# Kernel optimization log

Measured on AMD Instinct MI355X. Metric: run time of the kernel, lower is better.

## Reference

```python
import jax, jax.numpy as jnp
import numpy as np

N = 32768
WORD_DIM, TAG_DIM, REL_DIM, MEM_DIM, AT_HID = 300, 20, 20, 150, 20
IN_LEAF = WORD_DIM + TAG_DIM                      # 320, input to leaf SimpleGRU
IN_NODE = WORD_DIM + MEM_DIM + REL_DIM + TAG_DIM  # 490, input to GRU_AT


def _build_tree(seed=0):
    rng = np.random.default_rng(seed)
    parent = np.zeros(N, np.int64)
    for i in range(1, N):
        parent[i] = rng.integers(max(0, i - 64), i)
    children = [[] for _ in range(N)]
    for i in range(1, N):
        children[parent[i]].append(i)
    # Edge schedule: parents in DECREASING index order, children ascending.
    # Since child index > parent index, all edges below a node fire before
    # the node itself is consumed as a child => same order as the Python
    # post-order recursion in the torch code.
    edges = []
    for p in range(N - 1, -1, -1):
        for c in children[p]:
            edges.append((p, c))
    edges = np.asarray(edges, np.int32)            # (N-1, 2)
    leaf_ids = np.asarray([i for i in range(N) if not children[i]], np.int32)
    return edges, leaf_ids


def setup_inputs() -> dict:
    key = jax.random.key(0)
    ks = jax.random.split(key, 16)
    s = 0.05
    edges, leaf_ids = _build_tree()
    return {
        "w_emb":  jax.random.normal(ks[0], (N, WORD_DIM), jnp.float32),
        "tag_emb": jax.random.normal(ks[1], (N, TAG_DIM), jnp.float32),
        "rel_emb": jax.random.normal(ks[2], (N, REL_DIM), jnp.float32),
        "leaf_h": jax.random.uniform(ks[3], (MEM_DIM,), jnp.float32),
        # leaf SimpleGRU: stacked [Wz,Wr,Wh], [Uz,Ur,Uh], combined bias bW+bU
        "leaf_W": jax.random.normal(ks[4], (3, MEM_DIM, IN_LEAF), jnp.float32) * s,
        "leaf_U": jax.random.normal(ks[5], (3, MEM_DIM, MEM_DIM), jnp.float32) * s,
        "leaf_b": jax.random.normal(ks[6], (3, MEM_DIM), jnp.float32) * s,
        # GRU_AT inner SimpleGRU
        "node_W": jax.random.normal(ks[7], (3, MEM_DIM, IN_NODE), jnp.float32) * s,
        "node_U": jax.random.normal(ks[8], (3, MEM_DIM, MEM_DIM), jnp.float32) * s,
        "node_b": jax.random.normal(ks[9], (3, MEM_DIM), jnp.float32) * s,
        # attention gate AT: sigmoid(Wa tanh(Wb x + bb) + ba)
        "at_Wb": jax.random.normal(ks[10], (AT_HID, IN_NODE), jnp.float32) * s,
        "at_bb": jax.random.normal(ks[11], (AT_HID,), jnp.float32) * s,
        "at_Wa": jax.random.normal(ks[12], (AT_HID,), jnp.float32) * s,
        "at_ba": jax.random.normal(ks[13], (), jnp.float32) * s,
        "edges": jnp.asarray(edges),
        "leaf_ids": jnp.asarray(leaf_ids),
    }


def _simple_gru(W, U, b, x, h):
    # z = s(Wz x + Uz h + b); r = s(...); ht = tanh(...)
    # h_new = r*h + (1-z)*ht   (as written in the torch code)
    pre = jnp.einsum('kmi,i->km', W, x) + jnp.einsum('kmn,n->km', U, h) + b
    z = jax.nn.sigmoid(pre[0])
    r = jax.nn.sigmoid(pre[1])
    ht = jnp.tanh(pre[2])
    return r * h + (1.0 - z) * ht


def reference(w_emb, tag_emb, rel_emb, leaf_h,
              leaf_W, leaf_U, leaf_b,
              node_W, node_U, node_b,
              at_Wb, at_bb, at_Wa, at_ba,
              edges, leaf_ids):
    n, mem = w_emb.shape[0], leaf_h.shape[0]

    # ---- leaves (vectorized: all leaves share leaf_h, no dependencies) ----
    Xl = jnp.concatenate([w_emb[leaf_ids], tag_emb[leaf_ids]], axis=1)  # (L, IN_LEAF)
    pre = (jnp.einsum('kmi,li->lkm', leaf_W, Xl)
           + jnp.einsum('kmn,n->km', leaf_U, leaf_h)[None]
           + leaf_b[None])                                              # (L,3,mem)
    z = jax.nn.sigmoid(pre[:, 0])
    r = jax.nn.sigmoid(pre[:, 1])
    ht = jnp.tanh(pre[:, 2])
    k_leaf = r * leaf_h[None] + (1.0 - z) * ht                          # (L, mem)

    K = jnp.zeros((n, mem), w_emb.dtype).at[leaf_ids].set(k_leaf)  # node states k
    H = jnp.zeros((n, mem), w_emb.dtype)                           # per-node running h

    # ---- inner nodes: one GRU_AT step per (parent, child) edge ----
    def step(carry, pc):
        K, H = carry
        p, c = pc[0], pc[1]
        # x = cat([word_emb[p], k_child, rel_emb[child], tag_emb[p]])
        x = jnp.concatenate([w_emb[p], K[c], rel_emb[c], tag_emb[p]])
        h = H[p]
        m = _simple_gru(node_W, node_U, node_b, x, h)
        a = jax.nn.sigmoid(jnp.dot(at_Wa, jnp.tanh(at_Wb @ x + at_bb)) + at_ba)
        h_new = a * m + (1.0 - a) * h
        return (K.at[p].set(h_new), H.at[p].set(h_new)), None

    (K, H), _ = jax.lax.scan(step, (K, H), edges)
    return K[0]  # root state, (mem,)


if __name__ == '__main__':
    out = reference(**setup_inputs())
    print(out.shape, out.dtype)
```

## Files before the change

kernel.cpp:

```cpp
#include <hip/hip_runtime.h>
#include <hip/hip_fp16.h>
#include <stdint.h>


#define ROWS 470
#define AST  480
#define WST  512
#define NP2  76
#define KST  80
#define NPAIR 75

static __device__ __forceinline__ float fdot2f(uint32_t w, uint32_t x, float acc){
#if __has_builtin(__builtin_amdgcn_fdot2)
  typedef _Float16 h2v __attribute__((ext_vector_type(2)));
  return __builtin_amdgcn_fdot2(__builtin_bit_cast(h2v,w), __builtin_bit_cast(h2v,x), acc, false);
#else
  __half2 a = __builtin_bit_cast(__half2,w), b = __builtin_bit_cast(__half2,x);
  return acc + __low2float(a)*__low2float(b) + __high2float(a)*__high2float(b);
#endif
}
static __device__ __forceinline__ uint4 ld4(const uint32_t* __restrict__ P, int t, int q){
  return make_uint4(P[(4*q+0)*WST+t], P[(4*q+1)*WST+t], P[(4*q+2)*WST+t], P[(4*q+3)*WST+t]);
}
static __device__ __forceinline__ void pinu4(uint4 &v){
  asm volatile("" : "+v"(v.x), "+v"(v.y), "+v"(v.z), "+v"(v.w));
}
static __device__ __forceinline__ float sigm(float x){ return 1.f/(1.f+__expf(-x)); }
static __device__ __forceinline__ float tanhx(float x){ float e=__expf(2.f*x); return 1.f - 2.f/(e+1.f); }
static __device__ __forceinline__ uint32_t packh(float a, float b){
  return (uint32_t)__half_as_ushort(__float2half(a)) | ((uint32_t)__half_as_ushort(__float2half(b))<<16);
}
static __device__ __forceinline__ uint32_t aloadw(const uint32_t* p){
  return __hip_atomic_load(p, __ATOMIC_RELAXED, __HIP_MEMORY_SCOPE_AGENT);
}
static __device__ __forceinline__ void astoreh(unsigned short* p, unsigned short v){
  __hip_atomic_store(p, v, __ATOMIC_RELAXED, __HIP_MEMORY_SCOPE_AGENT);
}
static __device__ __forceinline__ bool validw(uint32_t w){
  return ((w & 0xffffu) != 0xffffu) && ((w >> 16) != 0xffffu);
}

#define DECL_W(W, P) \
  uint4 W##0=ld4(P,t,0),  W##1=ld4(P,t,1),  W##2=ld4(P,t,2),  W##3=ld4(P,t,3), \
        W##4=ld4(P,t,4),  W##5=ld4(P,t,5),  W##6=ld4(P,t,6),  W##7=ld4(P,t,7), \
        W##8=ld4(P,t,8),  W##9=ld4(P,t,9),  W##10=ld4(P,t,10),W##11=ld4(P,t,11), \
        W##12=ld4(P,t,12),W##13=ld4(P,t,13),W##14=ld4(P,t,14),W##15=ld4(P,t,15), \
        W##16=ld4(P,t,16),W##17=ld4(P,t,17),W##18=ld4(P,t,18);

#define PIN_W(W) \
  pinu4(W##0);  pinu4(W##1);  pinu4(W##2);  pinu4(W##3);  pinu4(W##4); \
  pinu4(W##5);  pinu4(W##6);  pinu4(W##7);  pinu4(W##8);  pinu4(W##9); \
  pinu4(W##10); pinu4(W##11); pinu4(W##12); pinu4(W##13); pinu4(W##14); \
  pinu4(W##15); pinu4(W##16); pinu4(W##17); pinu4(W##18);

#define DOT1(I, W, S) \
  _a0 = fdot2f(W##I.x, S[I].x, _a0); _a1 = fdot2f(W##I.y, S[I].y, _a1); \
  _a2 = fdot2f(W##I.z, S[I].z, _a2); _a3 = fdot2f(W##I.w, S[I].w, _a3);

#define DOT_ALL(P, W, S) { \
  float _a0 = 0.f, _a1 = 0.f, _a2 = 0.f, _a3 = 0.f; \
  DOT1(0,W,S)  DOT1(1,W,S)  DOT1(2,W,S)  DOT1(3,W,S)  DOT1(4,W,S) \
  DOT1(5,W,S)  DOT1(6,W,S)  DOT1(7,W,S)  DOT1(8,W,S)  DOT1(9,W,S) \
  DOT1(10,W,S) DOT1(11,W,S) DOT1(12,W,S) DOT1(13,W,S) DOT1(14,W,S) \
  DOT1(15,W,S) DOT1(16,W,S) DOT1(17,W,S) DOT1(18,W,S) \
  P = (P) + ((_a0 + _a1) + (_a2 + _a3)); \
}

#define DO_STEP(PRE, SRC, PUBP, OUTP, SLOT) { \
  float _pre = (PRE); \
  const uint4* _s4 = (const uint4*)(SRC); \
  DOT_ALL(_pre, wk, _s4); \
  if (rowOK) act[t] = (t < 300) ? sigm(_pre) : tanhx(_pre); \
  __syncthreads(); \
  if (t < 150) { \
    float _s = atba_v; \
    _Pragma("unroll") \
    for (int _j = 0; _j < 20; ++_j) _s += was[_j]*act[450 + _j]; \
    float _a = sigm(_s); \
    float _z = act[t], _r = act[150 + t], _ht = act[300 + t]; \
    float _m  = _r*hreg + (1.f - _z)*_ht; \
    float _hn = _a*_m + (1.f - _a)*hreg; \
    hreg = _hn; \
    unsigned short _hb = __half_as_ushort(__float2half(_hn)); \
    ((unsigned short*)h_pack)[t] = _hb; \
    unsigned short* _pp = (PUBP); \
    if (_pp) astoreh(_pp + t, _hb); \
    float* _op = (OUTP); \
    if (_op) _op[t] = _hn; \
  } \
  if ((SLOT) >= 0 && t == 256) vstaged[(SLOT)] = 0; \
  __syncthreads(); \
}

#define CALC_UH(OUT) { \
  float _x = 0.f; \
  const uint4* _h4 = (const uint4*)h_pack; \
  DOT_ALL(_x, uw, _h4); \
  OUT = _x; \
}

__global__ void k_prep(const int* __restrict__ edges, int E,
                       const float* __restrict__ node_U, const float* __restrict__ node_W,
                       const float* __restrict__ at_Wb,  const float* __restrict__ leaf_W,
                       uint32_t* __restrict__ UW, uint32_t* __restrict__ WK,
                       float* __restrict__ NWT, float* __restrict__ LWT, float* __restrict__ RWT,
                       int* __restrict__ parent_of, int* __restrict__ has_child)
{
  int o = blockIdx.x*blockDim.x + threadIdx.x;
  if (o < E) {
    int p = edges[2*o], c = edges[2*o+1];
    parent_of[c] = p; has_child[p] = 1;
    if (o == 0) parent_of[0] = -1;
    return;
  }
  o -= E;
  if (o < NP2*WST) {
    int i = o/WST, j = o%WST;
    uint32_t v = 0u;
    if (i < NPAIR && j < 450) v = packh(node_U[j*150 + 2*i], node_U[j*150 + 2*i + 1]);
    UW[o] = v; return;
  }
  o -= NP2*WST;
  if (o < NP2*WST) {
    int i = o/WST, j = o%WST;
    uint32_t v = 0u;
    if (i < NPAIR) {
      if (j < 450)      v = packh(node_W[j*490 + 300 + 2*i], node_W[j*490 + 301 + 2*i]);
      else if (j < 470) v = packh(at_Wb[(j-450)*490 + 300 + 2*i], at_Wb[(j-450)*490 + 301 + 2*i]);
    }
    WK[o] = v; return;
  }
  o -= NP2*WST;
  if (o < 320*ROWS) {
    int i = o/ROWS, r = o%ROWS;
    int col = (i < 300) ? i : 470 + (i - 300);
    NWT[o] = (r < 450) ? node_W[r*490 + col] : at_Wb[(r-450)*490 + col];
    return;
  }
  o -= 320*ROWS;
  if (o < 320*450) {
    int i = o/450, r = o%450;
    LWT[o] = leaf_W[r*320 + i];
    return;
  }
  o -= 320*450;
  if (o < 20*ROWS) {
    int i = o/ROWS, r = o%ROWS;
    RWT[o] = (r < 450) ? node_W[r*490 + 450 + i] : at_Wb[(r-450)*490 + 450 + i];
    return;
  }
}

__global__ void k_uhleaf(const float* __restrict__ leaf_U, const float* __restrict__ leaf_h,
                         const float* __restrict__ leaf_b, float* __restrict__ uh_leaf)
{
  int t = threadIdx.x;
  if (t < 450) {
    float s = leaf_b[t];
    for (int n = 0; n < 150; ++n) s += leaf_U[t*150 + n]*leaf_h[n];
    uh_leaf[t] = s;
  }
}

__global__ void k_scan(const int* __restrict__ edges, int E,
                       int* __restrict__ group_start, int* __restrict__ ctrl,
                       int* __restrict__ node_group)
{
  __shared__ int warp_cnt[16];
  __shared__ int wbase[16];
  __shared__ int base_s;
  int t = threadIdx.x;
  if (t == 0) base_s = 0;
  __syncthreads();
  for (int chunk = 0; chunk < E; chunk += 1024) {
    int i = chunk + t;
    bool flag = false;
    if (i < E) flag = (i == 0) || (edges[2*(i-1)] != edges[2*i]);
    unsigned long long m = __ballot(flag ? 1 : 0);
    int wave = t >> 6, lane = t & 63;
    if (lane == 0) warp_cnt[wave] = __popcll(m);
    __syncthreads();
    if (t == 0) {
      int run = base_s;
      for (int w = 0; w < 16; ++w) { wbase[w] = run; run += warp_cnt[w]; }
      base_s = run;
    }
    __syncthreads();
    if (flag) {
      int g = wbase[wave] + __popcll(m & ((1ull << lane) - 1ull));
      group_start[g] = i;
    }
    __syncthreads();
  }
  if (t == 0) { ctrl[1] = base_s; group_start[base_s] = E; }
  __syncthreads();
  int NG = base_s;
  for (int g = t; g < NG; g += 1024) node_group[edges[2*group_start[g]]] = g;
}

__global__ void k_leaf(const int* __restrict__ leaf_ids,
                       const float* __restrict__ w_emb, const float* __restrict__ tag_emb,
                       const float* __restrict__ LWT, const float* __restrict__ uh_leaf,
                       const float* __restrict__ leaf_h,
                       uint32_t* __restrict__ K_pack, int L)
{
  int base = blockIdx.x*8; if (base >= L) return;
  int cnt = min(8, L - base);
  __shared__ __align__(16) float xs[320*8];
  __shared__ float actl[8*450];
  __shared__ int lid[8];
  __shared__ float lh[150];
  int t = threadIdx.x;
  if (t < cnt) lid[t] = leaf_ids[base + t];
  if (t < 150) lh[t] = leaf_h[t];
  __syncthreads();
  for (int idx = t; idx < cnt*320; idx += 512) {
    int nl = idx/320, i = idx%320; int n = lid[nl];
    xs[i*8 + nl] = (i < 300) ? w_emb[(size_t)n*300 + i] : tag_emb[(size_t)n*20 + (i-300)];
  }
  __syncthreads();
  if (t < 450) {
    float a0=0,a1=0,a2=0,a3=0,a4=0,a5=0,a6=0,a7=0;
    for (int i = 0; i < 320; ++i) {
      float w = LWT[i*450 + t];
      const float4* x4 = (const float4*)(xs + i*8);
      float4 xa = x4[0], xb = x4[1];
      a0 += w*xa.x; a1 += w*xa.y; a2 += w*xa.z; a3 += w*xa.w;
      a4 += w*xb.x; a5 += w*xb.y; a6 += w*xb.z; a7 += w*xb.w;
    }
    float acc[8] = {a0,a1,a2,a3,a4,a5,a6,a7};
    float uh = uh_leaf[t];
    for (int j = 0; j < cnt; ++j) {
      float pre = acc[j] + uh;
      actl[j*450 + t] = (t < 300) ? sigm(pre) : tanhx(pre);
    }
  }
  __syncthreads();
  for (int idx = t; idx < cnt*150; idx += 512) {
    int nl = idx/150, m = idx%150;
    float z = actl[nl*450 + m], r = actl[nl*450 + 150 + m], ht = actl[nl*450 + 300 + m];
    float kv = r*lh[m] + (1.f - z)*ht;
    ((unsigned short*)(K_pack + (size_t)lid[nl]*KST))[m] = __half_as_ushort(__float2half(kv));
  }
}

__global__ void k_static(const int* __restrict__ edges, const int* __restrict__ group_start,
                         const int* __restrict__ ctrl,
                         const float* __restrict__ w_emb, const float* __restrict__ tag_emb,
                         const float* __restrict__ NWT, const float* __restrict__ node_b,
                         const float* __restrict__ at_bb, __half* __restrict__ A_all)
{
  int NG = ctrl[1];
  int base = blockIdx.x*16; if (base >= NG) return;
  int cnt = min(16, NG - base);
  __shared__ __align__(16) float xs[320*16];
  __shared__ int pl[16];
  int t = threadIdx.x;
  if (t < cnt) pl[t] = edges[2*group_start[base + t]];
  __syncthreads();
  for (int idx = t; idx < cnt*320; idx += 512) {
    int nl = idx/320, i = idx%320; int n = pl[nl];
    xs[i*16 + nl] = (i < 300) ? w_emb[(size_t)n*300 + i] : tag_emb[(size_t)n*20 + (i-300)];
  }
  __syncthreads();
  if (t < ROWS) {
    float acc[16];
    #pragma unroll
    for (int j = 0; j < 16; ++j) acc[j] = 0.f;
    for (int i = 0; i < 320; ++i) {
      float w = NWT[i*ROWS + t];
      const float4* x4 = (const float4*)(xs + i*16);
      float4 xa = x4[0], xb = x4[1], xc = x4[2], xd = x4[3];
      acc[0]+=w*xa.x; acc[1]+=w*xa.y; acc[2]+=w*xa.z; acc[3]+=w*xa.w;
      acc[4]+=w*xb.x; acc[5]+=w*xb.y; acc[6]+=w*xb.z; acc[7]+=w*xb.w;
      acc[8]+=w*xc.x; acc[9]+=w*xc.y; acc[10]+=w*xc.z; acc[11]+=w*xc.w;
      acc[12]+=w*xd.x; acc[13]+=w*xd.y; acc[14]+=w*xd.z; acc[15]+=w*xd.w;
    }
    float bias = (t < 450) ? node_b[t] : at_bb[t-450];
    for (int j = 0; j < cnt; ++j)
      A_all[(size_t)pl[j]*AST + t] = __float2half(acc[j] + bias);
  }
}

__global__ void k_rel(const float* __restrict__ rel_emb, const float* __restrict__ RWT_g,
                      __half* __restrict__ R_all, int N)
{
  __shared__ float rw[20*ROWS];
  __shared__ float xs[20*32];
  int t = threadIdx.x;
  for (int idx = t; idx < 20*ROWS; idx += 512) rw[idx] = RWT_g[idx];
  int base = blockIdx.x*32;
  int cnt = min(32, N - base);
  for (int idx = t; idx < cnt*20; idx += 512) {
    int nl = idx/20, i = idx%20;
    xs[i*32 + nl] = rel_emb[(size_t)(base+nl)*20 + i];
  }
  __syncthreads();
  if (t < ROWS) {
    float w[20];
    #pragma unroll
    for (int i = 0; i < 20; ++i) w[i] = rw[i*ROWS + t];
    for (int j = 0; j < cnt; ++j) {
      float acc = 0.f;
      #pragma unroll
      for (int i = 0; i < 20; ++i) acc += w[i]*xs[i*32 + j];
      R_all[(size_t)(base+j)*AST + t] = __float2half(acc);
    }
  }
}

__global__ __launch_bounds__(512, 1)
void k_worker(const int* __restrict__ edges,
              const float* __restrict__ at_Wa, const float* __restrict__ at_ba,
              const uint32_t* __restrict__ UW, const uint32_t* __restrict__ WK,
              const __half* __restrict__ A_all, const __half* __restrict__ R_all,
              uint32_t* __restrict__ K_pack,
              int* __restrict__ ctrl, const int* __restrict__ group_start,
              const int* __restrict__ parent_of, const int* __restrict__ node_group,
              const int* __restrict__ has_child, float* __restrict__ d_out)
{
  const int t = threadIdx.x;
  const bool rowOK = (t < ROWS);

  __shared__ __align__(16) uint32_t h_pack[80];
  __shared__ __align__(16) uint32_t kbuf[8*76];
  __shared__ float act[472];
  __shared__ float was[20];
  __shared__ int   s_g;
  volatile __shared__ int vstaged[8];

  DECL_W(wk, WK)
  DECL_W(uw, UW)
  PIN_W(wk)
  PIN_W(uw)

  if (t >= NPAIR && t < 80) h_pack[t] = 0u;
  if (t < 8) { vstaged[t] = 0; kbuf[t*76 + 75] = 0u; }
  if (t < 20) was[t] = at_Wa[t];
  const float atba_v = at_ba[0];
  const int NG = ctrl[1];
  float hreg = 0.f;
  __syncthreads();

  for (;;) {
    if (t == 0) s_g = atomicAdd(&ctrl[0], 1);
    __syncthreads();
    const int g = s_g;
    if (g >= NG) break;
    const int gs = group_start[g], ge = group_start[g+1];
    const int p  = edges[2*gs];
    if (ge - gs == 1 && has_child[edges[2*gs + 1]]) continue;

    int  r = parent_of[p];
    bool single = false;
    if (r >= 0) {
      const int gr = node_group[r];
      single = (group_start[gr+1] - group_start[gr] == 1);
    }
    const float aSt = rowOK ? __half2float(A_all[(size_t)p*AST + t]) : 0.f;
    float aN = 0.f, rN = 0.f;
    if (single && rowOK) {
      aN = __half2float(A_all[(size_t)r*AST + t]);
      rN = __half2float(R_all[(size_t)p*AST + t]);
    }
    if (t < 150) hreg = 0.f;
    float uh = 0.f;

    {
      const int w = t >> 6, l = t & 63;
      const int j = gs + w;
      if (w >= 1 && j < ge) {
        const int cj = edges[2*j + 1];
        const uint32_t* rowp = K_pack + (size_t)cj*KST;
        uint32_t a = aloadw(rowp + l);
        uint32_t b = (l < 11) ? aloadw(rowp + 64 + l) : 0u;
        bool ok = validw(a) && (l >= 11 || validw(b));
        if (__all(ok)) {
          uint32_t* kb = kbuf + w*76;
          kb[l] = a; if (l < 11) kb[64 + l] = b;
          if (l == 0) vstaged[w] = 1;
        }
      }
    }

    for (int e = gs; e < ge; ++e) {
      const int slot = (e - gs) & 7;
      const int c = edges[2*e + 1];
      const float rSt = rowOK ? __half2float(R_all[(size_t)c*AST + t]) : 0.f;
      {
        const int w = t >> 6, l = t & 63;
        if (w == 0 && !vstaged[slot]) {
          const uint32_t* rowp = K_pack + (size_t)c*KST;
          uint32_t* kb = kbuf + slot*76;
          long spins = 0;
          for (;;) {
            uint32_t a = aloadw(rowp + l);
            uint32_t b = (l < 11) ? aloadw(rowp + 64 + l) : 0u;
            bool ok = validw(a) && (l >= 11 || validw(b));
            if (__all(ok)) { kb[l] = a; if (l < 11) kb[64 + l] = b; break; }
            __builtin_amdgcn_s_sleep(1);
            if (++spins > 50000000L) break;
          }
        }
      }
      __syncthreads();
      unsigned short* pubp = nullptr; float* outp = nullptr;
      if (e + 1 == ge) {
        if (p == 0) outp = d_out;
        else if (!single) pubp = (unsigned short*)(K_pack + (size_t)p*KST);
      }
      DO_STEP(aSt + rSt + uh, kbuf + slot*76, pubp, outp, slot)
      if (e + 1 < ge) { CALC_UH(uh) } else uh = 0.f;
    }

    int q = p;
    for (;;) {
      if (q == 0) break;
      if (!single) break;
      const int r2p = parent_of[r];
      bool s2 = false;
      if (r2p >= 0) {
        const int gr2 = node_group[r2p];
        s2 = (group_start[gr2+1] - group_start[gr2] == 1);
      }
      float aN2 = 0.f, rN2 = 0.f;
      if (s2 && rowOK) {
        aN2 = __half2float(A_all[(size_t)r2p*AST + t]);
        rN2 = __half2float(R_all[(size_t)r*AST + t]);
      }
      if (t < 150) hreg = 0.f;
      unsigned short* pubp = nullptr; float* outp = nullptr;
      if (r == 0) outp = d_out;
      else if (!s2) pubp = (unsigned short*)(K_pack + (size_t)r*KST);
      DO_STEP(aN + rN, h_pack, pubp, outp, -1)
      q = r; r = r2p; single = s2; aN = aN2; rN = rN2;
    }
  }
}

extern "C" void kernel_launch(void* const* d_in, const int* in_sizes, int n_in,
                              void* d_out, int out_size, void* d_ws, size_t ws_size,
                              hipStream_t stream)
{
  const float* w_emb   = (const float*)d_in[0];
  const float* tag_emb = (const float*)d_in[1];
  const float* rel_emb = (const float*)d_in[2];
  const float* leaf_h  = (const float*)d_in[3];
  const float* leaf_W  = (const float*)d_in[4];
  const float* leaf_U  = (const float*)d_in[5];
  const float* leaf_b  = (const float*)d_in[6];
  const float* node_W  = (const float*)d_in[7];
  const float* node_U  = (const float*)d_in[8];
  const float* node_b  = (const float*)d_in[9];
  const float* at_Wb   = (const float*)d_in[10];
  const float* at_bb   = (const float*)d_in[11];
  const float* at_Wa   = (const float*)d_in[12];
  const float* at_ba   = (const float*)d_in[13];
  const int*   edges   = (const int*)d_in[14];
  const int*   leaf_ids= (const int*)d_in[15];
  float* out = (float*)d_out;

  const int N = in_sizes[0]/300;
  const int E = in_sizes[14]/2;
  const int L = in_sizes[15];

  char* ws = (char*)d_ws;
  size_t off = 0;
  auto take = [&](size_t bytes) -> char* {
    char* p = ws + off;
    off = (off + bytes + 255) & ~(size_t)255;
    return p;
  };
  size_t zbytes = 256 + (size_t)4*N;
  char* zbase       = take(zbytes);
  int*  ctrl        = (int*)zbase;
  int*  has_child   = (int*)(zbase + 256);
  int*  parent_of   = (int*)take((size_t)4*N);
  int*  node_group  = (int*)take((size_t)4*N);
  int*  group_start = (int*)take((size_t)4*(N+1));
  uint32_t* UW      = (uint32_t*)take((size_t)4*NP2*WST);
  uint32_t* WK      = (uint32_t*)take((size_t)4*NP2*WST);
  float* NWT        = (float*)take((size_t)4*320*ROWS);
  float* LWT        = (float*)take((size_t)4*320*450);
  float* RWT        = (float*)take((size_t)4*20*ROWS);
  float* uh_leaf    = (float*)take((size_t)4*456);
  __half* A_all     = (__half*)take((size_t)2*((size_t)N*AST + 64));
  __half* R_all     = (__half*)take((size_t)2*((size_t)N*AST + 64));
  uint32_t* K_pack  = (uint32_t*)take((size_t)4*(size_t)N*KST);
  (void)ws_size; (void)n_in; (void)out_size;

  hipMemsetAsync(zbase, 0, zbytes, stream);
  hipMemsetAsync(K_pack, 0xFF, (size_t)4*(size_t)N*KST, stream);

  const int TOT = E + NP2*WST + NP2*WST + 320*ROWS + 320*450 + 20*ROWS;
  k_prep<<<(TOT + 255)/256, 256, 0, stream>>>(edges, E, node_U, node_W, at_Wb, leaf_W,
                                              UW, WK, NWT, LWT, RWT, parent_of, has_child);
  k_uhleaf<<<1, 512, 0, stream>>>(leaf_U, leaf_h, leaf_b, uh_leaf);
  k_scan<<<1, 1024, 0, stream>>>(edges, E, group_start, ctrl, node_group);
  k_leaf<<<(L + 7)/8, 512, 0, stream>>>(leaf_ids, w_emb, tag_emb, LWT, uh_leaf, leaf_h,
                                        K_pack, L);
  k_static<<<(N + 15)/16, 512, 0, stream>>>(edges, group_start, ctrl, w_emb, tag_emb,
                                            NWT, node_b, at_bb, A_all);
  k_rel<<<(N + 31)/32, 512, 0, stream>>>(rel_emb, RWT, R_all, N);
  k_worker<<<256, 512, 0, stream>>>(edges, at_Wa, at_ba, UW, WK, A_all, R_all,
                                    K_pack, ctrl, group_start, parent_of,
                                    node_group, has_child, out);
}
```

Before: 2.684 ms.

## Partition worker queue by XCD region and add L2-local duplicate K buffer

Splits the group work queue into 8 node-index regions, each with its own counter, and assigns workgroups to start on the region matching blockIdx&7. The intent is to keep producer and consumer of child states on the same XCD. Child states are also written to a second buffer with plain stores and polled with sc0 loads, which are meant to hit the local L2. The agent-scope atomic buffer is checked every fourth spin as a fallback for cross-XCD producers. This adds extra writes, an extra memset and more polling traffic, and the ordering between the plain stores and the polling loads is relaxed.

Result: slower. 3.197 ms (+19.1%).

```diff
diff --git a/kernel.cpp b/kernel.cpp
--- a/kernel.cpp
+++ b/kernel.cpp
@@ -36,6 +36,16 @@
 static __device__ __forceinline__ void astoreh(unsigned short* p, unsigned short v){
   __hip_atomic_store(p, v, __ATOMIC_RELAXED, __HIP_MEMORY_SCOPE_AGENT);
 }
+static __device__ __forceinline__ void l2load2(const uint32_t* pa, const uint32_t* pb,
+                                               uint32_t &a, uint32_t &b){
+  asm volatile("global_load_dword %0, %2, off sc0\n\t"
+               "global_load_dword %1, %3, off sc0\n\t"
+               "s_waitcnt vmcnt(0)"
+               : "=&v"(a), "=&v"(b)
+               : "v"((unsigned long long)(uintptr_t)pa),
+                 "v"((unsigned long long)(uintptr_t)pb)
+               : "memory");
+}
 static __device__ __forceinline__ bool validw(uint32_t w){
   return ((w & 0xffffu) != 0xffffu) && ((w >> 16) != 0xffffu);
 }
@@ -66,7 +76,7 @@
   P = (P) + ((_a0 + _a1) + (_a2 + _a3)); \
 }
 
-#define DO_STEP(PRE, SRC, PUBP, OUTP, SLOT) { \
+#define DO_STEP(PRE, SRC, PUBP, PUBF, OUTP, SLOT) { \
   float _pre = (PRE); \
   const uint4* _s4 = (const uint4*)(SRC); \
   DOT_ALL(_pre, wk, _s4); \
@@ -83,6 +93,8 @@
     hreg = _hn; \
     unsigned short _hb = __half_as_ushort(__float2half(_hn)); \
     ((unsigned short*)h_pack)[t] = _hb; \
+    unsigned short* _pf = (PUBF); \
+    if (_pf) _pf[t] = _hb; \
     unsigned short* _pp = (PUBP); \
     if (_pp) astoreh(_pp + t, _hb); \
     float* _op = (OUTP); \
@@ -164,13 +176,16 @@
 
 __global__ void k_scan(const int* __restrict__ edges, int E,
                        int* __restrict__ group_start, int* __restrict__ ctrl,
-                       int* __restrict__ node_group)
+                       int* __restrict__ node_group,
+                       int* __restrict__ reg_lo, int* __restrict__ reg_hi, int Nn)
 {
   __shared__ int warp_cnt[16];
   __shared__ int wbase[16];
   __shared__ int base_s;
+  __shared__ int s_lo[8], s_hi[8];
   int t = threadIdx.x;
   if (t == 0) base_s = 0;
+  if (t < 8) { s_lo[t] = 0x7fffffff; s_hi[t] = -1; }
   __syncthreads();
   for (int chunk = 0; chunk < E; chunk += 1024) {
     int i = chunk + t;
@@ -195,14 +210,21 @@
   if (t == 0) { ctrl[1] = base_s; group_start[base_s] = E; }
   __syncthreads();
   int NG = base_s;
-  for (int g = t; g < NG; g += 1024) node_group[edges[2*group_start[g]]] = g;
+  for (int g = t; g < NG; g += 1024) {
+    int p = edges[2*group_start[g]];
+    node_group[p] = g;
+    int r = (int)(((long long)p * 8) / Nn);
+    atomicMin(&s_lo[r], g); atomicMax(&s_hi[r], g);
+  }
+  __syncthreads();
+  if (t < 8) { reg_lo[t] = s_lo[t]; reg_hi[t] = s_hi[t]; }
 }
 
 __global__ void k_leaf(const int* __restrict__ leaf_ids,
                        const float* __restrict__ w_emb, const float* __restrict__ tag_emb,
                        const float* __restrict__ LWT, const float* __restrict__ uh_leaf,
                        const float* __restrict__ leaf_h,
-                       uint32_t* __restrict__ K_pack, int L)
+                       uint32_t* __restrict__ K_pack, uint32_t* __restrict__ K_fast, int L)
 {
   int base = blockIdx.x*8; if (base >= L) return;
   int cnt = min(8, L - base);
@@ -240,7 +262,9 @@
     int nl = idx/150, m = idx%150;
     float z = actl[nl*450 + m], r = actl[nl*450 + 150 + m], ht = actl[nl*450 + 300 + m];
     float kv = r*lh[m] + (1.f - z)*ht;
-    ((unsigned short*)(K_pack + (size_t)lid[nl]*KST))[m] = __half_as_ushort(__float2half(kv));
+    unsigned short hb = __half_as_ushort(__float2half(kv));
+    ((unsigned short*)(K_pack + (size_t)lid[nl]*KST))[m] = hb;
+    ((unsigned short*)(K_fast + (size_t)lid[nl]*KST))[m] = hb;
   }
 }
 
@@ -314,10 +338,12 @@
               const float* __restrict__ at_Wa, const float* __restrict__ at_ba,
               const uint32_t* __restrict__ UW, const uint32_t* __restrict__ WK,
               const __half* __restrict__ A_all, const __half* __restrict__ R_all,
-              uint32_t* __restrict__ K_pack,
+              uint32_t* __restrict__ K_pack, uint32_t* __restrict__ K_fast,
               int* __restrict__ ctrl, const int* __restrict__ group_start,
               const int* __restrict__ parent_of, const int* __restrict__ node_group,
-              const int* __restrict__ has_child, float* __restrict__ d_out)
+              const int* __restrict__ has_child,
+              const int* __restrict__ reg_lo, const int* __restrict__ reg_hi,
+              float* __restrict__ d_out)
 {
   const int t = threadIdx.x;
   const bool rowOK = (t < ROWS);
@@ -338,102 +364,127 @@
   if (t < 8) { vstaged[t] = 0; kbuf[t*76 + 75] = 0u; }
   if (t < 20) was[t] = at_Wa[t];
   const float atba_v = at_ba[0];
-  const int NG = ctrl[1];
+  int* rc = ctrl + 8;
+  const int myreg = (int)(blockIdx.x & 7);
   float hreg = 0.f;
   __syncthreads();
 
-  for (;;) {
-    if (t == 0) s_g = atomicAdd(&ctrl[0], 1);
-    __syncthreads();
-    const int g = s_g;
-    if (g >= NG) break;
-    const int gs = group_start[g], ge = group_start[g+1];
-    const int p  = edges[2*gs];
-    if (ge - gs == 1 && has_child[edges[2*gs + 1]]) continue;
-
-    int  r = parent_of[p];
-    bool single = false;
-    if (r >= 0) {
-      const int gr = node_group[r];
-      single = (group_start[gr+1] - group_start[gr] == 1);
-    }
-    const float aSt = rowOK ? __half2float(A_all[(size_t)p*AST + t]) : 0.f;
-    float aN = 0.f, rN = 0.f;
-    if (single && rowOK) {
-      aN = __half2float(A_all[(size_t)r*AST + t]);
-      rN = __half2float(R_all[(size_t)p*AST + t]);
-    }
-    if (t < 150) hreg = 0.f;
-    float uh = 0.f;
-
-    {
-      const int w = t >> 6, l = t & 63;
-      const int j = gs + w;
-      if (w >= 1 && j < ge) {
-        const int cj = edges[2*j + 1];
-        const uint32_t* rowp = K_pack + (size_t)cj*KST;
-        uint32_t a = aloadw(rowp + l);
-        uint32_t b = (l < 11) ? aloadw(rowp + 64 + l) : 0u;
-        bool ok = validw(a) && (l >= 11 || validw(b));
-        if (__all(ok)) {
-          uint32_t* kb = kbuf + w*76;
-          kb[l] = a; if (l < 11) kb[64 + l] = b;
-          if (l == 0) vstaged[w] = 1;
-        }
+  for (int ord = 0; ord < 8; ++ord) {
+    const int rgn = (myreg + ord) & 7;
+    const int glo = reg_lo[rgn], ghi = reg_hi[rgn];
+    if (glo > ghi) continue;
+    for (;;) {
+      if (t == 0) s_g = glo + atomicAdd(&rc[rgn], 1);
+      __syncthreads();
+      const int g = s_g;
+      if (g > ghi) break;
+      const int gs = group_start[g], ge = group_start[g+1];
+      const int p  = edges[2*gs];
+      if (ge - gs == 1 && has_child[edges[2*gs + 1]]) continue;
+
+      int  r = parent_of[p];
+      bool single = false;
+      if (r >= 0) {
+        const int gr = node_group[r];
+        single = (group_start[gr+1] - group_start[gr] == 1);
       }
-    }
-
-    for (int e = gs; e < ge; ++e) {
-      const int slot = (e - gs) & 7;
-      const int c = edges[2*e + 1];
-      const float rSt = rowOK ? __half2float(R_all[(size_t)c*AST + t]) : 0.f;
+      const float aSt = rowOK ? __half2float(A_all[(size_t)p*AST + t]) : 0.f;
+      float aN = 0.f, rN = 0.f;
+      if (single && rowOK) {
+        aN = __half2float(A_all[(size_t)r*AST + t]);
+        rN = __half2float(R_all[(size_t)p*AST + t]);
+      }
+      if (t < 150) hreg = 0.f;
+      float uh = 0.f;
+
       {
         const int w = t >> 6, l = t & 63;
-        if (w == 0 && !vstaged[slot]) {
-          const uint32_t* rowp = K_pack + (size_t)c*KST;
-          uint32_t* kb = kbuf + slot*76;
-          long spins = 0;
-          for (;;) {
-            uint32_t a = aloadw(rowp + l);
-            uint32_t b = (l < 11) ? aloadw(rowp + 64 + l) : 0u;
-            bool ok = validw(a) && (l >= 11 || validw(b));
-            if (__all(ok)) { kb[l] = a; if (l < 11) kb[64 + l] = b; break; }
-            __builtin_amdgcn_s_sleep(1);
-            if (++spins > 50000000L) break;
+        const int j = gs + w;
+        if (w >= 1 && j < ge) {
+          const int cj = edges[2*j + 1];
+          const uint32_t* rowp = K_pack + (size_t)cj*KST;
+          uint32_t a = aloadw(rowp + l);
+          uint32_t b = (l < 11) ? aloadw(rowp + 64 + l) : 0u;
+          bool ok = validw(a) && (l >= 11 || validw(b));
+          if (__all(ok)) {
+            uint32_t* kb = kbuf + w*76;
+            kb[l] = a; if (l < 11) kb[64 + l] = b;
+            if (l == 0) vstaged[w] = 1;
           }
         }
       }
-      __syncthreads();
-      unsigned short* pubp = nullptr; float* outp = nullptr;
-      if (e + 1 == ge) {
-        if (p == 0) outp = d_out;
-        else if (!single) pubp = (unsigned short*)(K_pack + (size_t)p*KST);
+
+      for (int e = gs; e < ge; ++e) {
+        const int slot = (e - gs) & 7;
+        const int c = edges[2*e + 1];
+        const float rSt = rowOK ? __half2float(R_all[(size_t)c*AST + t]) : 0.f;
+        {
+          const int w = t >> 6, l = t & 63;
+          if (w == 0 && !vstaged[slot]) {
+            const uint32_t* rowf = K_fast + (size_t)c*KST;
+            const uint32_t* rows = K_pack + (size_t)c*KST;
+            uint32_t* kb = kbuf + slot*76;
+            const uint32_t* pa = rowf + l;
+            const uint32_t* pb = (l < 11) ? rowf + 64 + l : rowf + l;
+            long spins = 0;
+            for (;;) {
+              uint32_t a, b;
+              l2load2(pa, pb, a, b);
+              if (__all(validw(a) && (l >= 11 || validw(b)))) {
+                kb[l] = a; if (l < 11) kb[64 + l] = b; break;
+              }
+              if ((spins & 3) == 3) {
+                uint32_t as = aloadw(rows + l);
+                uint32_t bs = (l < 11) ? aloadw(rows + 64 + l) : 0u;
+                if (__all(validw(as) && (l >= 11 || validw(bs)))) {
+                  kb[l] = as; if (l < 11) kb[64 + l] = bs; break;
+                }
+              }
+              __builtin_amdgcn_s_sleep(1);
+              if (++spins > 50000000L) break;
+            }
+          }
+        }
+        __syncthreads();
+        unsigned short* pubp = nullptr; unsigned short* pubf = nullptr;
+        float* outp = nullptr;
+        if (e + 1 == ge) {
+          if (p == 0) outp = d_out;
+          else if (!single) {
+            pubp = (unsigned short*)(K_pack + (size_t)p*KST);
+            pubf = (unsigned short*)(K_fast + (size_t)p*KST);
+          }
+        }
+        DO_STEP(aSt + rSt + uh, kbuf + slot*76, pubp, pubf, outp, slot)
+        if (e + 1 < ge) { CALC_UH(uh) } else uh = 0.f;
       }
-      DO_STEP(aSt + rSt + uh, kbuf + slot*76, pubp, outp, slot)
-      if (e + 1 < ge) { CALC_UH(uh) } else uh = 0.f;
-    }
-
-    int q = p;
-    for (;;) {
-      if (q == 0) break;
-      if (!single) break;
-      const int r2p = parent_of[r];
-      bool s2 = false;
-      if (r2p >= 0) {
-        const int gr2 = node_group[r2p];
-        s2 = (group_start[gr2+1] - group_start[gr2] == 1);
+
+      int q = p;
+      for (;;) {
+        if (q == 0) break;
+        if (!single) break;
+        const int r2p = parent_of[r];
+        bool s2 = false;
+        if (r2p >= 0) {
+          const int gr2 = node_group[r2p];
+          s2 = (group_start[gr2+1] - group_start[gr2] == 1);
+        }
+        float aN2 = 0.f, rN2 = 0.f;
+        if (s2 && rowOK) {
+          aN2 = __half2float(A_all[(size_t)r2p*AST + t]);
+          rN2 = __half2float(R_all[(size_t)r*AST + t]);
+        }
+        if (t < 150) hreg = 0.f;
+        unsigned short* pubp = nullptr; unsigned short* pubf = nullptr;
+        float* outp = nullptr;
+        if (r == 0) outp = d_out;
+        else if (!s2) {
+          pubp = (unsigned short*)(K_pack + (size_t)r*KST);
+          pubf = (unsigned short*)(K_fast + (size_t)r*KST);
+        }
+        DO_STEP(aN + rN, h_pack, pubp, pubf, outp, -1)
+        q = r; r = r2p; single = s2; aN = aN2; rN = rN2;
       }
-      float aN2 = 0.f, rN2 = 0.f;
-      if (s2 && rowOK) {
-        aN2 = __half2float(A_all[(size_t)r2p*AST + t]);
-        rN2 = __half2float(R_all[(size_t)r*AST + t]);
-      }
-      if (t < 150) hreg = 0.f;
-      unsigned short* pubp = nullptr; float* outp = nullptr;
-      if (r == 0) outp = d_out;
-      else if (!s2) pubp = (unsigned short*)(K_pack + (size_t)r*KST);
-      DO_STEP(aN + rN, h_pack, pubp, outp, -1)
-      q = r; r = r2p; single = s2; aN = aN2; rN = rN2;
     }
   }
 }
@@ -478,6 +529,8 @@
   int*  parent_of   = (int*)take((size_t)4*N);
   int*  node_group  = (int*)take((size_t)4*N);
   int*  group_start = (int*)take((size_t)4*(N+1));
+  int*  reg_lo      = (int*)take(64);
+  int*  reg_hi      = (int*)take(64);
   uint32_t* UW      = (uint32_t*)take((size_t)4*NP2*WST);
   uint32_t* WK      = (uint32_t*)take((size_t)4*NP2*WST);
   float* NWT        = (float*)take((size_t)4*320*ROWS);
@@ -486,23 +539,26 @@
   float* uh_leaf    = (float*)take((size_t)4*456);
   __half* A_all     = (__half*)take((size_t)2*((size_t)N*AST + 64));
   __half* R_all     = (__half*)take((size_t)2*((size_t)N*AST + 64));
-  uint32_t* K_pack  = (uint32_t*)take((size_t)4*(size_t)N*KST);
+  uint32_t* K_pack  = (uint32_t*)take((size_t)4*((size_t)N*KST + 64));
+  uint32_t* K_fast  = (uint32_t*)take((size_t)4*((size_t)N*KST + 64));
   (void)ws_size; (void)n_in; (void)out_size;
 
   hipMemsetAsync(zbase, 0, zbytes, stream);
-  hipMemsetAsync(K_pack, 0xFF, (size_t)4*(size_t)N*KST, stream);
+  hipMemsetAsync(K_pack, 0xFF, (size_t)4*((size_t)N*KST + 64), stream);
+  hipMemsetAsync(K_fast, 0xFF, (size_t)4*((size_t)N*KST + 64), stream);
 
   const int TOT = E + NP2*WST + NP2*WST + 320*ROWS + 320*450 + 20*ROWS;
   k_prep<<<(TOT + 255)/256, 256, 0, stream>>>(edges, E, node_U, node_W, at_Wb, leaf_W,
                                               UW, WK, NWT, LWT, RWT, parent_of, has_child);
   k_uhleaf<<<1, 512, 0, stream>>>(leaf_U, leaf_h, leaf_b, uh_leaf);
-  k_scan<<<1, 1024, 0, stream>>>(edges, E, group_start, ctrl, node_group);
+  k_scan<<<1, 1024, 0, stream>>>(edges, E, group_start, ctrl, node_group,
+                                 reg_lo, reg_hi, N);
   k_leaf<<<(L + 7)/8, 512, 0, stream>>>(leaf_ids, w_emb, tag_emb, LWT, uh_leaf, leaf_h,
-                                        K_pack, L);
+                                        K_pack, K_fast, L);
   k_static<<<(N + 15)/16, 512, 0, stream>>>(edges, group_start, ctrl, w_emb, tag_emb,
                                             NWT, node_b, at_bb, A_all);
   k_rel<<<(N + 31)/32, 512, 0, stream>>>(rel_emb, RWT, R_all, N);
   k_worker<<<256, 512, 0, stream>>>(edges, at_Wa, at_ba, UW, WK, A_all, R_all,
-                                    K_pack, ctrl, group_start, parent_of,
-                                    node_group, has_child, out);
-}
+                                    K_pack, K_fast, ctrl, group_start, parent_of,
+                                    node_group, has_child, reg_lo, reg_hi, out);
+}
```
